# Kernel tuning notes

Hardware: AMD Instinct MI355X
Metric: run time of the kernel (lower is better)

## Reference

```python
import jax, jax.numpy as jnp
import numpy as np

N_NODES = 100000
N_EDGES = 1600000
N_GRAPHS = 64


def _sage(x, src, dst, Wl, bl, Wr):
    # SAGEConv (mean aggr): out = lin_l(mean_j x_j) + lin_r(x_i)
    msg = x[src]                                             # [E, F] gather
    s = jax.ops.segment_sum(msg, dst, num_segments=N_NODES)  # [N, F]
    cnt = jax.ops.segment_sum(jnp.ones((msg.shape[0],), x.dtype), dst,
                              num_segments=N_NODES)[:, None]
    mean = jnp.where(cnt > 0, s / jnp.maximum(cnt, 1.0), 0.0)
    return mean @ Wl + bl + x @ Wr


def setup_inputs() -> dict:
    key = jax.random.key(0)
    ks = jax.random.split(key, 12)
    sc = lambda f: 1.0 / np.sqrt(f)
    inp = {
        'x':   jax.random.normal(ks[0], (N_NODES, 32), jnp.float32),
        'Wl0': jax.random.normal(ks[1], (32, 64), jnp.float32) * sc(32),
        'bl0': jnp.zeros((64,), jnp.float32),
        'Wr0': jax.random.normal(ks[2], (32, 64), jnp.float32) * sc(32),
        'Wl1': jax.random.normal(ks[3], (64, 64), jnp.float32) * sc(64),
        'bl1': jnp.zeros((64,), jnp.float32),
        'Wr1': jax.random.normal(ks[4], (64, 64), jnp.float32) * sc(64),
        'Wl2': jax.random.normal(ks[5], (64, 64), jnp.float32) * sc(64),
        'bl2': jnp.zeros((64,), jnp.float32),
        'Wr2': jax.random.normal(ks[6], (64, 64), jnp.float32) * sc(64),
        'W_out': jax.random.normal(ks[7], (64, 8), jnp.float32) * sc(64),
        'b_out': jnp.zeros((8,), jnp.float32),
        'edge_index': jax.random.randint(ks[8], (2, N_EDGES), 0, N_NODES, jnp.int32),
        'batch': jnp.sort(jax.random.randint(ks[9], (N_NODES,), 0, N_GRAPHS, jnp.int32)),
    }
    return inp


def reference(x, Wl0, bl0, Wr0, Wl1, bl1, Wr1, Wl2, bl2, Wr2,
              W_out, b_out, edge_index, batch):
    src, dst = edge_index[0], edge_index[1]
    h = _sage(x, src, dst, Wl0, bl0, Wr0)
    h = _sage(h, src, dst, Wl1, bl1, Wr1)
    h = _sage(h, src, dst, Wl2, bl2, Wr2)
    pooled = jax.ops.segment_max(h, batch, num_segments=N_GRAPHS)  # [G, 64]
    logits = pooled @ W_out + b_out
    return jax.nn.log_softmax(logits, axis=-1)
```

## Files before the change

### kernel.cpp

```cpp
#include <hip/hip_runtime.h>
#include <math.h>
#include <stdint.h>

#define N_NODES 100000
#define N_EDGES 1600000
#define N_GRAPHS 64

#define BSH 9
#define NBKT 196
#define NCHUNK 256
#define EPC 6250
#define FLAT (NBKT * NCHUNK)


typedef __attribute__((ext_vector_type(8))) short bf16x8;
typedef __attribute__((ext_vector_type(8))) unsigned short u16x8;
typedef __attribute__((ext_vector_type(4))) float f32x4;

__device__ __forceinline__ void atomicMaxFloat(float* addr, float val) {
    if (val >= 0.0f) {
        atomicMax((int*)addr, __float_as_int(val));
    } else {
        atomicMin((unsigned int*)addr, __float_as_uint(val));
    }
}

__device__ __forceinline__ unsigned short f2bf(float f) {
    unsigned u = __float_as_uint(f);
    unsigned r = (u + 0x7FFFu + ((u >> 16) & 1u)) >> 16;
    return (unsigned short)r;
}
__device__ __forceinline__ float bf2f(unsigned short b) {
    return __uint_as_float(((unsigned)b) << 16);
}

__global__ __launch_bounds__(256) void k_prep(
    const float* __restrict__ x, unsigned short* __restrict__ xhi,
    const int* __restrict__ batch, int* __restrict__ gstart,
    float* __restrict__ pooled) {
    int i = blockIdx.x * blockDim.x + threadIdx.x;
    if (i < N_NODES * 32 / 8) {
        int base = i * 8;
        const float4* xp = (const float4*)(x + base);
        float4 a = xp[0], b = xp[1];
        u16x8 o;
        o[0] = f2bf(a.x); o[1] = f2bf(a.y); o[2] = f2bf(a.z); o[3] = f2bf(a.w);
        o[4] = f2bf(b.x); o[5] = f2bf(b.y); o[6] = f2bf(b.z); o[7] = f2bf(b.w);
        *(u16x8*)(xhi + base) = o;
    }
    if (i < N_GRAPHS * 64) pooled[i] = -INFINITY;
    if (i < N_NODES) {
        int b = batch[i];
        if (i == 0) {
            for (int g = 0; g <= b; ++g) gstart[g] = 0;
        } else {
            int pb = batch[i - 1];
            for (int g = pb + 1; g <= b; ++g) gstart[g] = i;
        }
        if (i == N_NODES - 1) {
            for (int g = b + 1; g <= N_GRAPHS; ++g) gstart[g] = N_NODES;
        }
    }
}

__global__ __launch_bounds__(256) void k_rhist(const int* __restrict__ dst,
                                               int* __restrict__ S) {
    __shared__ int h[NBKT];
    for (int i = threadIdx.x; i < NBKT; i += 256) h[i] = 0;
    __syncthreads();
    int c = blockIdx.x;
    int e0 = c * EPC;
    for (int e = e0 + threadIdx.x; e < e0 + EPC; e += 256)
        atomicAdd(&h[dst[e] >> BSH], 1);
    __syncthreads();
    for (int i = threadIdx.x; i < NBKT; i += 256) S[i * NCHUNK + c] = h[i];
}

__global__ __launch_bounds__(1024) void k_rscan(int* __restrict__ S) {
    __shared__ int part[1024];
    int t = threadIdx.x;
    const int seg = (FLAT + 1023) / 1024;
    int lo = t * seg;
    int hi = lo + seg; if (hi > FLAT) hi = FLAT;
    int s = 0;
    for (int i = lo; i < hi; ++i) s += S[i];
    part[t] = s;
    __syncthreads();
    for (int off = 1; off < 1024; off <<= 1) {
        int add = (t >= off) ? part[t - off] : 0;
        __syncthreads();
        part[t] += add;
        __syncthreads();
    }
    int ex = (t > 0) ? part[t - 1] : 0;
    if (t == 1023) S[FLAT] = part[1023];
    int run = ex;
    for (int i = lo; i < hi; ++i) { int v = S[i]; S[i] = run; run += v; }
}

__global__ __launch_bounds__(256) void k_rscatter(
    const int* __restrict__ src, const int* __restrict__ dst,
    const int* __restrict__ S, unsigned int* __restrict__ pairs) {
    __shared__ int ofs[NBKT];
    __shared__ int cnt[NBKT];
    int c = blockIdx.x;
    for (int i = threadIdx.x; i < NBKT; i += 256) {
        ofs[i] = S[i * NCHUNK + c];
        cnt[i] = 0;
    }
    __syncthreads();
    int e0 = c * EPC;
    for (int e = e0 + threadIdx.x; e < e0 + EPC; e += 256) {
        int d = dst[e];
        int b = d >> BSH;
        int r = atomicAdd(&cnt[b], 1);
        pairs[ofs[b] + r] = ((unsigned)(d & 511) << 17) | (unsigned)src[e];
    }
}

__global__ __launch_bounds__(256) void k_rbuild(
    const unsigned int* __restrict__ pairs, const int* __restrict__ S,
    int* __restrict__ row_ptr, int* __restrict__ col) {
    __shared__ int ncnt[512];
    __shared__ int nofs[512];
    __shared__ int part[256];
    int b = blockIdx.x;
    int t = threadIdx.x;
    int base = S[b * NCHUNK];
    int next = (b == NBKT - 1) ? S[FLAT] : S[(b + 1) * NCHUNK];
    int count = next - base;
    int nodeBase = b << BSH;

    ncnt[2 * t] = 0; ncnt[2 * t + 1] = 0;
    __syncthreads();
    for (int i = t; i < count; i += 256)
        atomicAdd(&ncnt[pairs[base + i] >> 17], 1);
    __syncthreads();
    int v0 = ncnt[2 * t], v1 = ncnt[2 * t + 1];
    part[t] = v0 + v1;
    __syncthreads();
    for (int off = 1; off < 256; off <<= 1) {
        int add = (t >= off) ? part[t - off] : 0;
        __syncthreads();
        part[t] += add;
        __syncthreads();
    }
    int ex = (t > 0) ? part[t - 1] : 0;
    nofs[2 * t] = ex;
    nofs[2 * t + 1] = ex + v0;
    ncnt[2 * t] = 0; ncnt[2 * t + 1] = 0;
    __syncthreads();
    for (int i = t; i < 512; i += 256) {
        int node = nodeBase + i;
        if (node < N_NODES) row_ptr[node] = base + nofs[i];
    }
    if (b == 0 && t == 0) row_ptr[N_NODES] = N_EDGES;
    for (int i = t; i < count; i += 256) {
        unsigned p = pairs[base + i];
        int li = p >> 17;
        int r = atomicAdd(&ncnt[li], 1);
        col[base + nofs[li] + r] = (int)(p & 0x1FFFFu);
    }
}

template <int KM, bool XBF, int KX, int XS, int OM>
__global__ __launch_bounds__(256) void k_sage_fused(
    const unsigned short* __restrict__ ghb,
    const float* x,
    const unsigned short* xhi, const unsigned short* xlo,
    const int* __restrict__ row_ptr, const int* __restrict__ col,
    const float* __restrict__ Wl, const float* __restrict__ bl,
    const float* __restrict__ Wr,
    unsigned short* ohi, unsigned short* olo) {
    __shared__ float amean[2][KM][17];

    int lane = threadIdx.x & 63;
    int wid  = threadIdx.x >> 6;
    int sl   = wid >> 1;
    int half = wid & 1;
    int strip = blockIdx.x * 2 + sl;
    int row0 = strip * 16;

    {
        constexpr int G = (KM == 64) ? 4 : 8;
        constexpr int LPR = 64 / G;
        int g  = lane / LPR;
        int fq = lane % LPR;
        int nodeBase = row0 + half * 8;
        int rp = row_ptr[nodeBase + (lane < 8 ? lane : 8)];

        for (int i = 0; i < 8; ++i) {
            int start = __shfl(rp, i);
            int end   = __shfl(rp, i + 1);
            float s0 = 0.0f, s1 = 0.0f, s2 = 0.0f, s3 = 0.0f;

            for (int eb = start; eb < end; eb += 64) {
                int n = end - eb; if (n > 64) n = 64;
                int c = (eb + lane < end) ? col[eb + lane] : 0;
                int j = 0;
                for (; j + 4 * G - 1 < n; j += 4 * G) {
                    int cA = __shfl(c, j + g);
                    int cB = __shfl(c, j + G + g);
                    int cC = __shfl(c, j + 2 * G + g);
                    int cD = __shfl(c, j + 3 * G + g);
                    ushort4 vA = *(const ushort4*)(ghb + (size_t)cA * KM + fq * 4);
                    ushort4 vB = *(const ushort4*)(ghb + (size_t)cB * KM + fq * 4);
                    ushort4 vC = *(const ushort4*)(ghb + (size_t)cC * KM + fq * 4);
                    ushort4 vD = *(const ushort4*)(ghb + (size_t)cD * KM + fq * 4);
                    s0 += (bf2f(vA.x) + bf2f(vB.x)) + (bf2f(vC.x) + bf2f(vD.x));
                    s1 += (bf2f(vA.y) + bf2f(vB.y)) + (bf2f(vC.y) + bf2f(vD.y));
                    s2 += (bf2f(vA.z) + bf2f(vB.z)) + (bf2f(vC.z) + bf2f(vD.z));
                    s3 += (bf2f(vA.w) + bf2f(vB.w)) + (bf2f(vC.w) + bf2f(vD.w));
                }
                for (; j + 2 * G - 1 < n; j += 2 * G) {
                    int cA = __shfl(c, j + g);
                    int cB = __shfl(c, j + G + g);
                    ushort4 vA = *(const ushort4*)(ghb + (size_t)cA * KM + fq * 4);
                    ushort4 vB = *(const ushort4*)(ghb + (size_t)cB * KM + fq * 4);
                    s0 += bf2f(vA.x) + bf2f(vB.x);
                    s1 += bf2f(vA.y) + bf2f(vB.y);
                    s2 += bf2f(vA.z) + bf2f(vB.z);
                    s3 += bf2f(vA.w) + bf2f(vB.w);
                }
                for (; j + G - 1 < n; j += G) {
                    int cA = __shfl(c, j + g);
                    ushort4 vA = *(const ushort4*)(ghb + (size_t)cA * KM + fq * 4);
                    s0 += bf2f(vA.x);
                    s1 += bf2f(vA.y);
                    s2 += bf2f(vA.z);
                    s3 += bf2f(vA.w);
                }
                if (j < n) {
                    int idx = j + g;
                    bool valid = idx < n;
                    int cA = __shfl(c, valid ? idx : 0);
                    ushort4 vA = *(const ushort4*)(ghb + (size_t)cA * KM + fq * 4);
                    if (valid) {
                        s0 += bf2f(vA.x);
                        s1 += bf2f(vA.y);
                        s2 += bf2f(vA.z);
                        s3 += bf2f(vA.w);
                    }
                }
            }
#pragma unroll
            for (int m = LPR; m < 64; m <<= 1) {
                s0 += __shfl_xor(s0, m);
                s1 += __shfl_xor(s1, m);
                s2 += __shfl_xor(s2, m);
                s3 += __shfl_xor(s3, m);
            }
            int deg = end - start;
            float inv = (deg > 0) ? 1.0f / (float)deg : 0.0f;
            if (lane < LPR) {
                int lr = half * 8 + i;
                amean[sl][fq * 4 + 0][lr] = s0 * inv;
                amean[sl][fq * 4 + 1][lr] = s1 * inv;
                amean[sl][fq * 4 + 2][lr] = s2 * inv;
                amean[sl][fq * 4 + 3][lr] = s3 * inv;
            }
        }
    }
    __syncthreads();

    int m = lane & 15;
    int g = lane >> 4;
    f32x4 acc[2] = {};

#pragma unroll
    for (int kt = 0; kt < KM / 32; ++kt) {
        int k0 = kt * 32 + g * 8;
        bf16x8 ahi, alo;
#pragma unroll
        for (int j = 0; j < 8; ++j) {
            float v = amean[sl][k0 + j][m];
            unsigned short hb = f2bf(v);
            ahi[j] = (short)hb;
            alo[j] = (short)f2bf(v - bf2f(hb));
        }
#pragma unroll
        for (int nti = 0; nti < 2; ++nti) {
            int nt = half * 2 + nti;
            bf16x8 b;
#pragma unroll
            for (int j = 0; j < 8; ++j)
                b[j] = (short)f2bf(Wl[(size_t)(k0 + j) * 64 + nt * 16 + m]);
            acc[nti] = __builtin_amdgcn_mfma_f32_16x16x32_bf16(ahi, b, acc[nti], 0, 0, 0);
            acc[nti] = __builtin_amdgcn_mfma_f32_16x16x32_bf16(alo, b, acc[nti], 0, 0, 0);
        }
    }
#pragma unroll
    for (int kt = 0; kt < KX / 32; ++kt) {
        int k0 = kt * 32 + g * 8;
        bf16x8 ahi, alo;
        if constexpr (XBF) {
            ahi = *(const bf16x8*)(xhi + (size_t)(row0 + m) * XS + k0);
            alo = *(const bf16x8*)(xlo + (size_t)(row0 + m) * XS + k0);
        } else {
            const float4* ap = (const float4*)(x + (size_t)(row0 + m) * XS + k0);
            float4 a0 = ap[0], a1 = ap[1];
            float av[8] = {a0.x, a0.y, a0.z, a0.w, a1.x, a1.y, a1.z, a1.w};
#pragma unroll
            for (int j = 0; j < 8; ++j) {
                unsigned short hb = f2bf(av[j]);
                ahi[j] = (short)hb;
                alo[j] = (short)f2bf(av[j] - bf2f(hb));
            }
        }
#pragma unroll
        for (int nti = 0; nti < 2; ++nti) {
            int nt = half * 2 + nti;
            bf16x8 b;
#pragma unroll
            for (int j = 0; j < 8; ++j)
                b[j] = (short)f2bf(Wr[(size_t)(k0 + j) * 64 + nt * 16 + m]);
            acc[nti] = __builtin_amdgcn_mfma_f32_16x16x32_bf16(ahi, b, acc[nti], 0, 0, 0);
            acc[nti] = __builtin_amdgcn_mfma_f32_16x16x32_bf16(alo, b, acc[nti], 0, 0, 0);
        }
    }
#pragma unroll
    for (int nti = 0; nti < 2; ++nti) {
        int nt = half * 2 + nti;
        float bias = bl[nt * 16 + m];
#pragma unroll
        for (int r = 0; r < 4; ++r) {
            int row = row0 + g * 4 + r;
            float v = acc[nti][r] + bias;
            if constexpr (OM == 1) {
                unsigned short hb = f2bf(v);
                ohi[(size_t)row * 64 + nt * 16 + m] = hb;
                olo[(size_t)row * 64 + nt * 16 + m] = f2bf(v - bf2f(hb));
            } else {
                ohi[(size_t)row * 64 + nt * 16 + m] = f2bf(v);
            }
        }
    }
}

#define PSPLIT 8
__global__ __launch_bounds__(256) void k_pool2(const unsigned short* __restrict__ h,
                                               const int* __restrict__ gstart,
                                               float* __restrict__ pooled) {
    __shared__ float red[4][64];
    int gr = blockIdx.x & 63;
    int split = blockIdx.x >> 6;
    int lane = threadIdx.x & 63;
    int w = threadIdx.x >> 6;
    int s = gstart[gr], e = gstart[gr + 1];
    float m = -INFINITY;
    for (int i = s + split * 4 + w; i < e; i += PSPLIT * 4)
        m = fmaxf(m, bf2f(h[(size_t)i * 64 + lane]));
    red[w][lane] = m;
    __syncthreads();
    if (w == 0) {
        m = fmaxf(fmaxf(red[0][lane], red[1][lane]),
                  fmaxf(red[2][lane], red[3][lane]));
        if (m > -INFINITY) atomicMaxFloat(&pooled[gr * 64 + lane], m);
    }
}

__global__ void k_head(const float* __restrict__ pooled,
                       const float* __restrict__ Wout,
                       const float* __restrict__ bout, float* __restrict__ out) {
    int tid = threadIdx.x;
    int g = tid >> 3, o = tid & 7;
    float acc = bout[o];
#pragma unroll
    for (int k = 0; k < 64; ++k) acc += pooled[g * 64 + k] * Wout[k * 8 + o];
    float mx = acc;
#pragma unroll
    for (int m = 1; m < 8; m <<= 1) mx = fmaxf(mx, __shfl_xor(mx, m));
    float ex = expf(acc - mx);
    float sum = ex;
#pragma unroll
    for (int m = 1; m < 8; m <<= 1) sum += __shfl_xor(sum, m);
    out[g * 8 + o] = (acc - mx) - logf(sum);
}

extern "C" void kernel_launch(void* const* d_in, const int* in_sizes, int n_in,
                              void* d_out, int out_size, void* d_ws, size_t ws_size,
                              hipStream_t stream) {
    const float* x    = (const float*)d_in[0];
    const float* Wl0  = (const float*)d_in[1];
    const float* bl0  = (const float*)d_in[2];
    const float* Wr0  = (const float*)d_in[3];
    const float* Wl1  = (const float*)d_in[4];
    const float* bl1  = (const float*)d_in[5];
    const float* Wr1  = (const float*)d_in[6];
    const float* Wl2  = (const float*)d_in[7];
    const float* bl2  = (const float*)d_in[8];
    const float* Wr2  = (const float*)d_in[9];
    const float* Wout = (const float*)d_in[10];
    const float* bout = (const float*)d_in[11];
    const int*   eidx = (const int*)d_in[12];
    const int*   batch= (const int*)d_in[13];
    const int* src = eidx;
    const int* dst = eidx + N_EDGES;

    uint8_t* ws = (uint8_t*)d_ws;
    int*   S       = (int*)(ws + 0);
    int*   row_ptr = (int*)(ws + 400128);
    int*   col     = (int*)(ws + 800256);
    float* pooled  = (float*)(ws + 7200384);
    int*   gstart  = (int*)(ws + 7216768);
    unsigned short* H1hi = (unsigned short*)(ws + 7217408);
    unsigned short* H1lo = (unsigned short*)(ws + 20017408);
    unsigned short* H2hi = (unsigned short*)(ws + 32817408);
    unsigned short* H2lo = (unsigned short*)(ws + 45617408);
    unsigned int* pairs  = (unsigned int*)(ws + 32817408);
    unsigned short* Xhi  = (unsigned short*)(ws + 45617408);

    k_prep<<<(N_NODES * 32 / 8 + 255) / 256, 256, 0, stream>>>(
        x, Xhi, batch, gstart, pooled);
    k_rhist<<<NCHUNK, 256, 0, stream>>>(dst, S);
    k_rscan<<<1, 1024, 0, stream>>>(S);
    k_rscatter<<<NCHUNK, 256, 0, stream>>>(src, dst, S, pairs);
    k_rbuild<<<NBKT, 256, 0, stream>>>(pairs, S, row_ptr, col);

    int fusedBlocks = N_NODES / 32;

    k_sage_fused<32, false, 32, 32, 1><<<fusedBlocks, 256, 0, stream>>>(
        Xhi, x, nullptr, nullptr, row_ptr, col, Wl0, bl0, Wr0, H1hi, H1lo);
    k_sage_fused<64, true, 64, 64, 1><<<fusedBlocks, 256, 0, stream>>>(
        H1hi, nullptr, H1hi, H1lo, row_ptr, col, Wl1, bl1, Wr1, H2hi, H2lo);
    k_sage_fused<64, true, 64, 64, 2><<<fusedBlocks, 256, 0, stream>>>(
        H2hi, nullptr, H2hi, H2lo, row_ptr, col, Wl2, bl2, Wr2, H1hi, nullptr);

    k_pool2<<<64 * PSPLIT, 256, 0, stream>>>(H1hi, gstart, pooled);
    k_head<<<1, 512, 0, stream>>>(pooled, Wout, bout, (float*)d_out);
}
```

Baseline: 238.4 us.

## Pre-transpose weights to bf16 once and merge histogram into prep kernel

Adds a one-time conversion of all six SAGE weight matrices to transposed bf16 in workspace inside the prep kernel. The fused layers can then load each B fragment as a single 16-byte vector instead of eight strided fp32 loads plus conversions per MFMA. The mean-aggregation shared buffer is transposed to row-major so the A operand is read with float4 loads. The radix histogram kernel is folded into k_prep, which removes one launch. The risk is that k_prep now has a block-conditional __syncthreads and extra work in its first blocks.

```diff
diff --git a/kernel.cpp b/kernel.cpp
--- a/kernel.cpp
+++ b/kernel.cpp
@@ -17,6 +17,13 @@
 typedef __attribute__((ext_vector_type(8))) unsigned short u16x8;
 typedef __attribute__((ext_vector_type(4))) float f32x4;
 
+#define WT0L 0
+#define WT0R 2048
+#define WT1L 4096
+#define WT1R 8192
+#define WT2L 12288
+#define WT2R 16384
+
 __device__ __forceinline__ void atomicMaxFloat(float* addr, float val) {
     if (val >= 0.0f) {
         atomicMax((int*)addr, __float_as_int(val));
@@ -37,8 +44,15 @@
 __global__ __launch_bounds__(256) void k_prep(
     const float* __restrict__ x, unsigned short* __restrict__ xhi,
     const int* __restrict__ batch, int* __restrict__ gstart,
-    float* __restrict__ pooled) {
+    float* __restrict__ pooled,
+    const float* __restrict__ Wl0, const float* __restrict__ Wr0,
+    const float* __restrict__ Wl1, const float* __restrict__ Wr1,
+    const float* __restrict__ Wl2, const float* __restrict__ Wr2,
+    unsigned short* __restrict__ WT,
+    const int* __restrict__ dst, int* __restrict__ S) {
+    __shared__ int h[NBKT];
     int i = blockIdx.x * blockDim.x + threadIdx.x;
+
     if (i < N_NODES * 32 / 8) {
         int base = i * 8;
         const float4* xp = (const float4*)(x + base);
@@ -61,19 +75,31 @@
             for (int g = b + 1; g <= N_GRAPHS; ++g) gstart[g] = N_NODES;
         }
     }
-}
-
-__global__ __launch_bounds__(256) void k_rhist(const int* __restrict__ dst,
-                                               int* __restrict__ S) {
-    __shared__ int h[NBKT];
-    for (int i = threadIdx.x; i < NBKT; i += 256) h[i] = 0;
-    __syncthreads();
-    int c = blockIdx.x;
-    int e0 = c * EPC;
-    for (int e = e0 + threadIdx.x; e < e0 + EPC; e += 256)
-        atomicAdd(&h[dst[e] >> BSH], 1);
-    __syncthreads();
-    for (int i = threadIdx.x; i < NBKT; i += 256) S[i * NCHUNK + c] = h[i];
+    if (i < 2560) {
+        const float* Wsrc; int wofs, KW, local;
+        if (i < 256)       { Wsrc = Wl0; wofs = WT0L; KW = 32; local = i; }
+        else if (i < 512)  { Wsrc = Wr0; wofs = WT0R; KW = 32; local = i - 256; }
+        else if (i < 1024) { Wsrc = Wl1; wofs = WT1L; KW = 64; local = i - 512; }
+        else if (i < 1536) { Wsrc = Wr1; wofs = WT1R; KW = 64; local = i - 1024; }
+        else if (i < 2048) { Wsrc = Wl2; wofs = WT2L; KW = 64; local = i - 1536; }
+        else               { Wsrc = Wr2; wofs = WT2R; KW = 64; local = i - 2048; }
+        int e = local * 8;
+        int colw = e / KW, k0 = e % KW;
+        u16x8 o;
+#pragma unroll
+        for (int j = 0; j < 8; ++j) o[j] = f2bf(Wsrc[(size_t)(k0 + j) * 64 + colw]);
+        *(u16x8*)(WT + wofs + e) = o;
+    }
+    if (blockIdx.x < NCHUNK) {
+        for (int q = threadIdx.x; q < NBKT; q += 256) h[q] = 0;
+        __syncthreads();
+        int c = blockIdx.x;
+        int e0 = c * EPC;
+        for (int e = e0 + threadIdx.x; e < e0 + EPC; e += 256)
+            atomicAdd(&h[dst[e] >> BSH], 1);
+        __syncthreads();
+        for (int q = threadIdx.x; q < NBKT; q += 256) S[q * NCHUNK + c] = h[q];
+    }
 }
 
 __global__ __launch_bounds__(1024) void k_rscan(int* __restrict__ S) {
@@ -169,10 +195,11 @@
     const float* x,
     const unsigned short* xhi, const unsigned short* xlo,
     const int* __restrict__ row_ptr, const int* __restrict__ col,
-    const float* __restrict__ Wl, const float* __restrict__ bl,
-    const float* __restrict__ Wr,
+    const unsigned short* __restrict__ WTl,
+    const float* __restrict__ bl,
+    const unsigned short* __restrict__ WTr,
     unsigned short* ohi, unsigned short* olo) {
-    __shared__ float amean[2][KM][17];
+    __shared__ float amean[2][16][KM + 4];
 
     int lane = threadIdx.x & 63;
     int wid  = threadIdx.x >> 6;
@@ -254,10 +281,8 @@
             float inv = (deg > 0) ? 1.0f / (float)deg : 0.0f;
             if (lane < LPR) {
                 int lr = half * 8 + i;
-                amean[sl][fq * 4 + 0][lr] = s0 * inv;
-                amean[sl][fq * 4 + 1][lr] = s1 * inv;
-                amean[sl][fq * 4 + 2][lr] = s2 * inv;
-                amean[sl][fq * 4 + 3][lr] = s3 * inv;
+                *(float4*)&amean[sl][lr][fq * 4] =
+                    make_float4(s0 * inv, s1 * inv, s2 * inv, s3 * inv);
             }
         }
     }
@@ -270,21 +295,21 @@
 #pragma unroll
     for (int kt = 0; kt < KM / 32; ++kt) {
         int k0 = kt * 32 + g * 8;
+        const float* ar = &amean[sl][m][k0];
+        float4 a0 = *(const float4*)(ar);
+        float4 a1 = *(const float4*)(ar + 4);
+        float av[8] = {a0.x, a0.y, a0.z, a0.w, a1.x, a1.y, a1.z, a1.w};
         bf16x8 ahi, alo;
 #pragma unroll
         for (int j = 0; j < 8; ++j) {
-            float v = amean[sl][k0 + j][m];
-            unsigned short hb = f2bf(v);
+            unsigned short hb = f2bf(av[j]);
             ahi[j] = (short)hb;
-            alo[j] = (short)f2bf(v - bf2f(hb));
+            alo[j] = (short)f2bf(av[j] - bf2f(hb));
         }
 #pragma unroll
         for (int nti = 0; nti < 2; ++nti) {
             int nt = half * 2 + nti;
-            bf16x8 b;
-#pragma unroll
-            for (int j = 0; j < 8; ++j)
-                b[j] = (short)f2bf(Wl[(size_t)(k0 + j) * 64 + nt * 16 + m]);
+            bf16x8 b = *(const bf16x8*)(WTl + (size_t)(nt * 16 + m) * KM + k0);
             acc[nti] = __builtin_amdgcn_mfma_f32_16x16x32_bf16(ahi, b, acc[nti], 0, 0, 0);
             acc[nti] = __builtin_amdgcn_mfma_f32_16x16x32_bf16(alo, b, acc[nti], 0, 0, 0);
         }
@@ -310,10 +335,7 @@
 #pragma unroll
         for (int nti = 0; nti < 2; ++nti) {
             int nt = half * 2 + nti;
-            bf16x8 b;
-#pragma unroll
-            for (int j = 0; j < 8; ++j)
-                b[j] = (short)f2bf(Wr[(size_t)(k0 + j) * 64 + nt * 16 + m]);
+            bf16x8 b = *(const bf16x8*)(WTr + (size_t)(nt * 16 + m) * KX + k0);
             acc[nti] = __builtin_amdgcn_mfma_f32_16x16x32_bf16(ahi, b, acc[nti], 0, 0, 0);
             acc[nti] = __builtin_amdgcn_mfma_f32_16x16x32_bf16(alo, b, acc[nti], 0, 0, 0);
         }
@@ -399,6 +421,7 @@
 
     uint8_t* ws = (uint8_t*)d_ws;
     int*   S       = (int*)(ws + 0);
+    unsigned short* WT = (unsigned short*)(ws + 204800);
     int*   row_ptr = (int*)(ws + 400128);
     int*   col     = (int*)(ws + 800256);
     float* pooled  = (float*)(ws + 7200384);
@@ -411,8 +434,8 @@
     unsigned short* Xhi  = (unsigned short*)(ws + 45617408);
 
     k_prep<<<(N_NODES * 32 / 8 + 255) / 256, 256, 0, stream>>>(
-        x, Xhi, batch, gstart, pooled);
-    k_rhist<<<NCHUNK, 256, 0, stream>>>(dst, S);
+        x, Xhi, batch, gstart, pooled,
+        Wl0, Wr0, Wl1, Wr1, Wl2, Wr2, WT, dst, S);
     k_rscan<<<1, 1024, 0, stream>>>(S);
     k_rscatter<<<NCHUNK, 256, 0, stream>>>(src, dst, S, pairs);
     k_rbuild<<<NBKT, 256, 0, stream>>>(pairs, S, row_ptr, col);
@@ -420,11 +443,14 @@
     int fusedBlocks = N_NODES / 32;
 
     k_sage_fused<32, false, 32, 32, 1><<<fusedBlocks, 256, 0, stream>>>(
-        Xhi, x, nullptr, nullptr, row_ptr, col, Wl0, bl0, Wr0, H1hi, H1lo);
+        Xhi, x, nullptr, nullptr, row_ptr, col,
+        WT + WT0L, bl0, WT + WT0R, H1hi, H1lo);
     k_sage_fused<64, true, 64, 64, 1><<<fusedBlocks, 256, 0, stream>>>(
-        H1hi, nullptr, H1hi, H1lo, row_ptr, col, Wl1, bl1, Wr1, H2hi, H2lo);
+        H1hi, nullptr, H1hi, H1lo, row_ptr, col,
+        WT + WT1L, bl1, WT + WT1R, H2hi, H2lo);
     k_sage_fused<64, true, 64, 64, 2><<<fusedBlocks, 256, 0, stream>>>(
-        H2hi, nullptr, H2hi, H2lo, row_ptr, col, Wl2, bl2, Wr2, H1hi, nullptr);
+        H2hi, nullptr, H2hi, H2lo, row_ptr, col,
+        WT + WT2L, bl2, WT + WT2R, H1hi, nullptr);
 
     k_pool2<<<64 * PSPLIT, 256, 0, stream>>>(H1hi, gstart, pooled);
     k_head<<<1, 512, 0, stream>>>(pooled, Wout, bout, (float*)d_out);
```

After: 222.8 us (median of 2 runs). 6.5% less time.
